# Kernel tuning notes

Hardware: AMD Instinct MI355X
Metric: run time of the kernel (lower is better)

The kernel has to match this reference:

```python
import jax, jax.numpy as jnp
import numpy as np

B, T, D = 8, 4096, 768

def setup_inputs() -> dict:
    key = jax.random.key(0)
    k1, k2, k3, k4, k5, k6 = jax.random.split(key, 6)
    inputs = jax.random.normal(k1, (B, T, D), dtype=jnp.float32)
    mask = jax.random.randint(k2, (B, T), 0, 2, dtype=jnp.int32)
    s = 1.0 / np.sqrt(D)
    Wq_w = jax.random.normal(k3, (D, D), dtype=jnp.float32) * s
    Wq_b = jax.random.normal(k4, (D,), dtype=jnp.float32) * 0.02
    Wk_w = jax.random.normal(k5, (D, D), dtype=jnp.float32) * s
    Wk_b = jax.random.normal(k6, (D,), dtype=jnp.float32) * 0.02
    return {"inputs": inputs, "mask": mask, "Wq_w": Wq_w, "Wq_b": Wq_b, "Wk_w": Wk_w, "Wk_b": Wk_b}

def reference(inputs, mask, Wq_w, Wq_b, Wk_w, Wk_b):
    # Linear layers (torch: x @ W.T + b)
    query = jnp.einsum('btd,ed->bte', inputs, Wq_w) + Wq_b  # (b,t,d)
    key = jnp.einsum('btd,ed->bte', inputs, Wk_w) + Wk_b    # (b,t,d)
    d_k = query.shape[-1]
    scores = jnp.einsum('bqd,bkd->bqk', query, key) / jnp.sqrt(jnp.float32(d_k))  # (b,t,t)
    # mask.unsqueeze(1): (b,1,t) broadcast over query rows
    scores = jnp.where(mask[:, None, :] == 0, jnp.float32(-1e9), scores)
    weights = jax.nn.softmax(scores, axis=2)  # (b,t,t)
    # einsum 'btd,btt->bd' == diagonal of weights, weighted sum of inputs
    w_diag = jnp.einsum('btt->bt', weights)   # (b,t)
    outputs = jnp.einsum('btd,bt->bd', inputs, w_diag)  # (b,d)
    return outputs
```

## Files before the change

### kernel.cpp

```cpp
#include <hip/hip_runtime.h>

#define BB 8
#define TT 4096
#define DD 768
#define MM (BB*TT)

typedef _Float16 f16;
typedef _Float16 f16x8 __attribute__((ext_vector_type(8)));
typedef float f32x4 __attribute__((ext_vector_type(4)));

typedef __attribute__((address_space(1))) void void_g;
typedef __attribute__((address_space(3))) void void_l;

__device__ __forceinline__ void gload16(const void* g, void* l) {
  __builtin_amdgcn_global_load_lds((void_g*)g, (void_l*)l, 16, 0, 0);
}

__global__ __launch_bounds__(256)
void compact_mask(const int* __restrict__ mask, int* __restrict__ idx,
                  int* __restrict__ nbv) {
  __shared__ int wcnt[4];
  const int b = blockIdx.x;
  const int w = threadIdx.x >> 6, l = threadIdx.x & 63;
  const int* mb = mask + b * TT + w * 1024;
  int mv[16];
  unsigned long long bal[16];
#pragma unroll
  for (int c = 0; c < 16; ++c) {
    mv[c] = mb[c * 64 + l];
    bal[c] = __ballot(mv[c] != 0);
  }
  int tot = 0;
#pragma unroll
  for (int c = 0; c < 16; ++c) tot += __popcll(bal[c]);
  if (l == 0) wcnt[w] = tot;
  __syncthreads();
  int base = 0;
  for (int ww = 0; ww < w; ++ww) base += wcnt[ww];
#pragma unroll
  for (int c = 0; c < 16; ++c) {
    const int pre = __popcll(bal[c] & ((1ull << l) - 1ull));
    if (mv[c]) idx[b * TT + base + pre] = w * 1024 + c * 64 + l;
    base += __popcll(bal[c]);
  }
  if (w == 3 && l == 0) nbv[b] = base;
}

__global__ __launch_bounds__(256)
void cvt2T(const float* __restrict__ a, const float* __restrict__ b,
           f16* __restrict__ oaT, f16* __restrict__ obT) {
  __shared__ float tile[64][65];
  const float* src = blockIdx.z ? b : a;
  f16* dst = blockIdx.z ? obT : oaT;
  const int n0 = blockIdx.x * 64, d0 = blockIdx.y * 64;
  const int r = threadIdx.x >> 6, c = threadIdx.x & 63;
#pragma unroll
  for (int k = 0; k < 16; ++k)
    tile[k * 4 + r][c] = src[(size_t)(n0 + k * 4 + r) * DD + d0 + c];
  __syncthreads();
#pragma unroll
  for (int k = 0; k < 16; ++k)
    dst[(size_t)(d0 + k * 4 + r) * DD + n0 + c] = (f16)tile[c][k * 4 + r];
}

__global__ __launch_bounds__(256)
void evec_k(const float* __restrict__ Wk, const float* __restrict__ bq,
            float* __restrict__ e) {
  const int d = blockIdx.x * 256 + threadIdx.x;
  float acc = 0.f;
  for (int n = 0; n < DD; ++n) acc += bq[n] * Wk[(size_t)n * DD + d];
  e[d] = acc;
}

__global__ __launch_bounds__(256)
void gather_cvt2(const float* __restrict__ X, const int* __restrict__ idx,
                 const int* __restrict__ nbv, const float* __restrict__ e,
                 f16* __restrict__ Xc, float* __restrict__ vb) {
  const int rr = blockIdx.x * 8 + (threadIdx.x >> 5);
  const int b = rr >> 12, j = rr & 4095;
  const int l = threadIdx.x & 31;
  if (j >= nbv[b]) return;
  const float scale = 0.036084391824351613f;
  const float* src = X + ((size_t)b * TT + idx[b * TT + j]) * DD + l * 24;
  f16* dst = Xc + ((size_t)b * TT + j) * DD + l * 24;
  const float* ep = e + l * 24;
  float vp = 0.f;
#pragma unroll
  for (int c = 0; c < 3; ++c) {
    float4 a = *(const float4*)(src + c * 8);
    float4 d4 = *(const float4*)(src + c * 8 + 4);
    f16x8 o;
    o[0] = (f16)a.x;  o[1] = (f16)a.y;  o[2] = (f16)a.z;  o[3] = (f16)a.w;
    o[4] = (f16)d4.x; o[5] = (f16)d4.y; o[6] = (f16)d4.z; o[7] = (f16)d4.w;
    *(f16x8*)(dst + c * 8) = o;
    vp += a.x * ep[c * 8]     + a.y * ep[c * 8 + 1] +
          a.z * ep[c * 8 + 2] + a.w * ep[c * 8 + 3] +
          d4.x * ep[c * 8 + 4] + d4.y * ep[c * 8 + 5] +
          d4.z * ep[c * 8 + 6] + d4.w * ep[c * 8 + 7];
  }
#pragma unroll
  for (int off = 1; off < 32; off <<= 1) vp += __shfl_xor(vp, off);
  if (l == 0) vb[b * TT + j] = vp * scale;
}

__global__ __launch_bounds__(256, 3)
void gemm_mt(const f16* __restrict__ WkT, const f16* __restrict__ WqT,
             f16* __restrict__ MT) {
  __shared__ f16 As[2][64 * 32];
  __shared__ f16 Ws[2][256 * 32];
  const int m0 = blockIdx.x * 64;
  const int n0 = blockIdx.y * 256;
  const int t = threadIdx.x;
  const int lane = t & 63;
  const int w = t >> 6;
  const int wn = w * 64;
  const int fr = lane & 15, fq = lane >> 4;
  const int xrd = ((fr >> 1) & 3) << 3;

  f32x4 acc[4][4] = {};

  const int r0 = t >> 2;
  const int c8 = ((t & 3) ^ ((t >> 3) & 3)) * 8;
  const f16* w0 = WqT + (size_t)(n0 + r0) * DD + c8;
  const f16* a0 = WkT + (size_t)(m0 + r0) * DD + c8;

#define PSTAGE(bf, ks_) do { \
    const int k0_ = (ks_) * 32; \
    gload16(a0 + k0_,                      &As[bf][w * 512]); \
    gload16(w0 + k0_,                      &Ws[bf][w * 512]); \
    gload16(w0 + (size_t)64  * DD + k0_,   &Ws[bf][2048 + w * 512]); \
    gload16(w0 + (size_t)128 * DD + k0_,   &Ws[bf][4096 + w * 512]); \
    gload16(w0 + (size_t)192 * DD + k0_,   &Ws[bf][6144 + w * 512]); \
  } while (0)

  PSTAGE(0, 0);
  __syncthreads();
  for (int ks = 0; ks < 24; ++ks) {
    const int bf = ks & 1;
    if (ks + 1 < 24) PSTAGE(bf ^ 1, ks + 1);
    f16x8 a[4], bfr[4];
#pragma unroll
    for (int i = 0; i < 4; ++i)
      a[i] = *(const f16x8*)&As[bf][(((i * 16 + fr) * 32) + fq * 8) ^ xrd];
#pragma unroll
    for (int j = 0; j < 4; ++j)
      bfr[j] = *(const f16x8*)&Ws[bf][(((wn + j * 16 + fr) * 32) + fq * 8) ^ xrd];
#pragma unroll
    for (int i = 0; i < 4; ++i)
#pragma unroll
      for (int j = 0; j < 4; ++j)
        acc[i][j] = __builtin_amdgcn_mfma_f32_16x16x32_f16(a[i], bfr[j], acc[i][j], 0, 0, 0);
    __syncthreads();
  }
#undef PSTAGE

#pragma unroll
  for (int j = 0; j < 4; ++j) {
    const int col = n0 + wn + j * 16 + fr;
#pragma unroll
    for (int i = 0; i < 4; ++i)
#pragma unroll
      for (int r = 0; r < 4; ++r) {
        const int row = m0 + i * 16 + fq * 4 + r;
        MT[(size_t)row * DD + col] = (f16)acc[i][j][r];
      }
  }
}

__global__ __launch_bounds__(256, 2)
void projY(const f16* __restrict__ Xc, const f16* __restrict__ MT,
           const int* __restrict__ nbv, f16* __restrict__ Yf) {
  const int b  = blockIdx.x >> 6;
  const int m0 = (blockIdx.x & 63) * 64;
  const int nb = nbv[b];
  if (m0 >= ((nb + 63) & ~63)) return;

  __shared__ f16 As[4][64 * 32];
  __shared__ f16 Ws[4][256 * 32];
  const int n0 = blockIdx.y * 256;
  const int t = threadIdx.x;
  const int lane = t & 63;
  const int w = t >> 6;
  const int wn = w * 64;
  const int fr = lane & 15, fq = lane >> 4;
  const int xrd = ((fr >> 1) & 3) << 3;

  f32x4 acc[4][4] = {};

  const int r0 = t >> 2;
  const int c8 = ((t & 3) ^ ((t >> 3) & 3)) * 8;
  const f16* w0 = MT + (size_t)(n0 + r0) * DD + c8;
  const f16* a0 = Xc + (size_t)b * TT * DD + (size_t)(m0 + r0) * DD + c8;

#define PSTAGE(sl, ks_) do { \
    const int k0_ = (ks_) * 32; \
    gload16(a0 + k0_,                      &As[sl][w * 512]); \
    gload16(w0 + k0_,                      &Ws[sl][w * 512]); \
    gload16(w0 + (size_t)64  * DD + k0_,   &Ws[sl][2048 + w * 512]); \
    gload16(w0 + (size_t)128 * DD + k0_,   &Ws[sl][4096 + w * 512]); \
    gload16(w0 + (size_t)192 * DD + k0_,   &Ws[sl][6144 + w * 512]); \
  } while (0)

  PSTAGE(0, 0);
  PSTAGE(1, 1);
  asm volatile("s_waitcnt vmcnt(5)" ::: "memory");
  __builtin_amdgcn_sched_barrier(0);
  __builtin_amdgcn_s_barrier();

  for (int ks = 0; ks < 24; ++ks) {
    const int sl = ks & 3;
    if (ks + 2 < 24) {
      PSTAGE((ks + 2) & 3, ks + 2);
      asm volatile("s_waitcnt vmcnt(10)" ::: "memory");
    } else if (ks + 1 < 24) {
      asm volatile("s_waitcnt vmcnt(5)" ::: "memory");
    } else {
      asm volatile("s_waitcnt vmcnt(0)" ::: "memory");
    }
    __builtin_amdgcn_sched_barrier(0);
    __builtin_amdgcn_s_barrier();
    __builtin_amdgcn_sched_barrier(0);

    f16x8 a[4], bfr[4];
#pragma unroll
    for (int i = 0; i < 4; ++i)
      a[i] = *(const f16x8*)&As[sl][(((i * 16 + fr) * 32) + fq * 8) ^ xrd];
#pragma unroll
    for (int j = 0; j < 4; ++j)
      bfr[j] = *(const f16x8*)&Ws[sl][(((wn + j * 16 + fr) * 32) + fq * 8) ^ xrd];
    __builtin_amdgcn_s_setprio(1);
#pragma unroll
    for (int i = 0; i < 4; ++i)
#pragma unroll
      for (int j = 0; j < 4; ++j)
        acc[i][j] = __builtin_amdgcn_mfma_f32_16x16x32_f16(a[i], bfr[j], acc[i][j], 0, 0, 0);
    __builtin_amdgcn_s_setprio(0);
    __builtin_amdgcn_sched_barrier(0);
    __builtin_amdgcn_s_barrier();
  }
#undef PSTAGE

#pragma unroll
  for (int j = 0; j < 4; ++j) {
    const int col = n0 + wn + j * 16 + fr;
#pragma unroll
    for (int i = 0; i < 4; ++i) {
#pragma unroll
      for (int r = 0; r < 4; ++r) {
        const int rowc = m0 + i * 16 + fq * 4 + r;
        const size_t q = (size_t)b * TT * DD +
            ((((size_t)(rowc >> 6) * 24 + (col >> 5)) * 4 + ((rowc >> 4) & 3)) * 512 +
             ((rowc & 15) + (((col >> 3) & 3) << 4)) * 8 + (col & 7));
        Yf[q] = (f16)acc[i][j][r];
      }
    }
  }
}

__global__ __launch_bounds__(256, 3)
void attn17b(const f16* __restrict__ Qf, const f16* __restrict__ K,
             const float* __restrict__ vbias, const int* __restrict__ nbv,
             float* __restrict__ pzv, float* __restrict__ sdg) {
  const int bid = blockIdx.x;
  const int qs = bid / 48;
  const int rem = bid % 48;
  const int kh = rem >> 3;
  const int bb = rem & 7;
  const int nb = nbv[bb];
  if (qs * 128 >= nb) return;

  __shared__ f16 Ks[2][128 * 64];
  const int t = threadIdx.x, l = t & 63, w = t >> 6;
  const int wq = w >> 1, wk = w & 1;
  const int fr = l & 15, fq = l >> 4;
  const int q0 = qs * 128;
  const float scale = 0.036084391824351613f;
  const int nkt = (nb + 127) >> 7;
  const int q6 = nkt / 6, r6 = nkt % 6;
  const int cnt = q6 + (kh < r6 ? 1 : 0);
  const int lo  = kh * q6 + (kh < r6 ? kh : r6);
  const int P = cnt * 12;

  const f16* Kg = K + (size_t)bb * TT * DD;
  const f16* qf = Qf + (size_t)bb * TT * DD + (size_t)(qs * 2 + wq) * 49152 + (size_t)l * 8;
  const float* vbp = vbias + bb * TT;

  const int c8 = ((t & 3) ^ ((t >> 3) & 3)) * 8;
  const f16* klo = Kg + (size_t)(t >> 2) * DD + c8;
  const f16* khi = klo + (size_t)64 * DD;

  const int sx = (fq ^ ((fr >> 1) & 3)) * 8;
  const int bbase = (wk * 64 + fr) * 32 + sx;

  f32x4 acc[4][4] = {};
  f32x4 zacc[4] = {};
  int im0 = 0, im1 = 0, im2 = 0, im3 = 0;
  float vb0 = 0.f, vb1 = 0.f, vb2 = 0.f, vb3 = 0.f;
  f16x8 avA[4], avB[4];

#define STAGE(bf, p_) do { \
    const size_t o0 = (size_t)(lo + (p_) / 12) * 128 * DD + (size_t)(((p_) % 12) * 64); \
    gload16(klo + o0,      &Ks[bf][w * 512]); \
    gload16(khi + o0,      &Ks[bf][2048 + w * 512]); \
    gload16(klo + o0 + 32, &Ks[bf][4096 + w * 512]); \
    gload16(khi + o0 + 32, &Ks[bf][6144 + w * 512]); \
  } while (0)

#define QLOAD(dst, dc_) do { \
    const f16* qp_ = qf + (size_t)(dc_) * 2048; \
    _Pragma("unroll") \
    for (int i = 0; i < 4; ++i) (dst)[i] = *(const f16x8*)(qp_ + i * 512); \
  } while (0)

#define MFMA_ALL(av_, bufv, off_) do { \
    f16x8 bv[4]; \
    _Pragma("unroll") \
    for (int j = 0; j < 4; ++j) bv[j] = *(const f16x8*)&Ks[bufv][(off_) + bbase + j * 512]; \
    __builtin_amdgcn_s_setprio(1); \
    _Pragma("unroll") \
    for (int i = 0; i < 4; ++i) \
      _Pragma("unroll") \
      for (int j = 0; j < 4; ++j) \
        acc[i][j] = __builtin_amdgcn_mfma_f32_16x16x32_f16((av_)[i], bv[j], acc[i][j], 0, 0, 0); \
    __builtin_amdgcn_s_setprio(0); \
  } while (0)

#define KT_EPILOGUE(kt_) do { \
    const float mb0 = im0 ? vb0 : -1e30f; \
    const float mb1 = im1 ? vb1 : -1e30f; \
    const float mb2 = im2 ? vb2 : -1e30f; \
    const float mb3 = im3 ? vb3 : -1e30f; \
    const bool isdiag = ((kt_) == qs); \
    _Pragma("unroll") \
    for (int i = 0; i < 4; ++i) { \
      _Pragma("unroll") \
      for (int rg = 0; rg < 4; ++rg) { \
        float v0 = fmaf(acc[i][0][rg], scale, mb0); \
        float v1 = fmaf(acc[i][1][rg], scale, mb1); \
        float v2 = fmaf(acc[i][2][rg], scale, mb2); \
        float v3 = fmaf(acc[i][3][rg], scale, mb3); \
        if (isdiag) { \
          const int rl = wq * 64 + i * 16 + fq * 4 + rg; \
          const int cl = wk * 64 + fr; \
          if (cl      == rl) sdg[(size_t)bb * TT + q0 + rl] = v0; \
          if (cl + 16 == rl) sdg[(size_t)bb * TT + q0 + rl] = v1; \
          if (cl + 32 == rl) sdg[(size_t)bb * TT + q0 + rl] = v2; \
          if (cl + 48 == rl) sdg[(size_t)bb * TT + q0 + rl] = v3; \
        } \
        zacc[i][rg] += __expf(v0) + __expf(v1) + __expf(v2) + __expf(v3); \
      } \
    } \
    _Pragma("unroll") \
    for (int i = 0; i < 4; ++i) \
      _Pragma("unroll") \
      for (int j = 0; j < 4; ++j) acc[i][j] = (f32x4)(0.f); \
  } while (0)

  STAGE(0, 0);
  QLOAD(avA, 0);
  __syncthreads();

  for (int p = 0; p < P; ++p) {
    const int buf = p & 1;
    const int kt = lo + p / 12, c = p % 12;
    if (c == 0) {
      const int cb0 = kt * 128 + wk * 64 + fr;
      im0 = (cb0 < nb); im1 = (cb0 + 16 < nb);
      im2 = (cb0 + 32 < nb); im3 = (cb0 + 48 < nb);
      vb0 = vbp[cb0]; vb1 = vbp[cb0 + 16];
      vb2 = vbp[cb0 + 32]; vb3 = vbp[cb0 + 48];
    }

    QLOAD(avB, 2 * c + 1);
    if (p + 1 < P) STAGE(buf ^ 1, p + 1);
    MFMA_ALL(avA, buf, 0);

    if (p + 1 < P) QLOAD(avA, 2 * (((p + 1) % 12)));
    MFMA_ALL(avB, buf, 4096);

    if (c == 11) KT_EPILOGUE(kt);

    __syncthreads();
  }
#undef STAGE
#undef QLOAD
#undef MFMA_ALL
#undef KT_EPILOGUE

  const int slot = kh * 2 + wk;
#pragma unroll
  for (int i = 0; i < 4; ++i) {
#pragma unroll
    for (int rg = 0; rg < 4; ++rg) {
      float z = zacc[i][rg];
#pragma unroll
      for (int off = 1; off < 16; off <<= 1) z += __shfl_xor(z, off);
      if (fr == 0) {
        const int row = wq * 64 + i * 16 + fq * 4 + rg;
        pzv[(size_t)slot * MM + bb * TT + q0 + row] = z;
      }
    }
  }
}

__global__ void merge12c(const float* __restrict__ pz, const float* __restrict__ sdg,
                         const int* __restrict__ nbv,
                         float* __restrict__ wdiagc, float* __restrict__ out) {
  int i = blockIdx.x * 256 + threadIdx.x;
  if (i < BB * DD) out[i] = 0.f;
  if (i >= MM) return;
  const int b = i >> 12, j = i & 4095;
  if (j >= nbv[b]) { wdiagc[i] = 0.f; return; }
  float Z = 0.f;
#pragma unroll
  for (int s = 0; s < 12; ++s) Z += pz[(size_t)s * MM + i];
  wdiagc[i] = __expf(sdg[i]) / Z;
}

__global__ __launch_bounds__(256)
void out_gemv_c(const f16* __restrict__ Xc, const float* __restrict__ wdiagc,
                const int* __restrict__ nbv, float* __restrict__ out) {
  __shared__ float wsm[256];
  const int b = blockIdx.z;
  const int nb = nbv[b];
  const int tbase = blockIdx.x * 256;
  if (tbase >= nb) return;
  const int d = blockIdx.y * 256 + threadIdx.x;
  wsm[threadIdx.x] = (tbase + threadIdx.x < nb) ? wdiagc[b * TT + tbase + threadIdx.x] : 0.f;
  __syncthreads();
  float acc = 0.f;
  const f16* xp = Xc + (size_t)(b * TT + tbase) * DD + d;
  const int lim = (nb - tbase < 256) ? (nb - tbase) : 256;
  for (int i = 0; i < lim; ++i) acc += (float)xp[(size_t)i * DD] * wsm[i];
  atomicAdd(&out[b * DD + d], acc);
}

extern "C" void kernel_launch(void* const* d_in, const int* in_sizes, int n_in,
                              void* d_out, int out_size, void* d_ws, size_t ws_size,
                              hipStream_t stream) {
  const float* X    = (const float*)d_in[0];
  const int*   mask = (const int*)d_in[1];
  const float* Wq_w = (const float*)d_in[2];
  const float* Wq_b = (const float*)d_in[3];
  const float* Wk_w = (const float*)d_in[4];
  const float* Wk_b = (const float*)d_in[5];
  float* out = (float*)d_out;

  const size_t n2 = (size_t)MM * DD;
  const size_t wde = (size_t)DD * DD;

  char* p = (char*)d_ws;
  f16* Yf  = (f16*)p;           p += n2 * sizeof(f16);
  f16* Xc  = (f16*)p;           p += n2 * sizeof(f16);
  f16* WqT = (f16*)p;           p += wde * sizeof(f16);
  f16* WkT = (f16*)p;           p += wde * sizeof(f16);
  f16* MT  = (f16*)p;           p += wde * sizeof(f16);
  float* ev = (float*)p;        p += DD * sizeof(float);
  int* idx = (int*)p;           p += (size_t)MM * sizeof(int);
  int* nbv = (int*)p;           p += 64;
  float* vb = (float*)p;        p += (size_t)MM * sizeof(float);
  float* pz = (float*)p;        p += (size_t)12 * MM * sizeof(float);
  float* sdg = (float*)p;       p += (size_t)MM * sizeof(float);
  float* wdiagc = (float*)p;    p += (size_t)MM * sizeof(float);

  compact_mask<<<8, 256, 0, stream>>>(mask, idx, nbv);
  cvt2T<<<dim3(12, 12, 2), 256, 0, stream>>>(Wq_w, Wk_w, WqT, WkT);
  evec_k<<<3, 256, 0, stream>>>(Wk_w, Wq_b, ev);
  gather_cvt2<<<4096, 256, 0, stream>>>(X, idx, nbv, ev, Xc, vb);
  gemm_mt<<<dim3(12, 3), 256, 0, stream>>>(WkT, WqT, MT);
  projY<<<dim3(512, 3), 256, 0, stream>>>(Xc, MT, nbv, Yf);
  attn17b<<<1536, 256, 0, stream>>>(Yf, Xc, vb, nbv, pz, sdg);
  merge12c<<<128, 256, 0, stream>>>(pz, sdg, nbv, wdiagc, out);
  out_gemv_c<<<dim3(16, 3, 8), 256, 0, stream>>>(Xc, wdiagc, nbv, out);
}
```

Baseline: 261.4 us.

## Merge prep kernels into fewer launches and simplify projY to double buffering

Folds the bias-vector GEMV into the mask-compaction kernel and the weight transpose into the gather/convert kernel, cutting four small launches down to two. projY drops from a 4-slot, 2-ahead prefetch pipeline with manual waitcnt and setprio to a plain 2-buffer scheme with __syncthreads, and raises its occupancy hint from 2 to 3 blocks. The fewer launches remove launch gaps. The simpler pipeline gives less latency hiding in exchange for lower LDS use and higher occupancy.

```diff
diff --git a/kernel.cpp b/kernel.cpp
--- a/kernel.cpp
+++ b/kernel.cpp
@@ -17,8 +17,16 @@
 }
 
 __global__ __launch_bounds__(256)
-void compact_mask(const int* __restrict__ mask, int* __restrict__ idx,
-                  int* __restrict__ nbv) {
+void compact_evec(const int* __restrict__ mask, int* __restrict__ idx,
+                  int* __restrict__ nbv, const float* __restrict__ Wk,
+                  const float* __restrict__ bq, float* __restrict__ e) {
+  if (blockIdx.x >= 8) {
+    const int d = (blockIdx.x - 8) * 256 + threadIdx.x;
+    float acc = 0.f;
+    for (int n = 0; n < DD; ++n) acc += bq[n] * Wk[(size_t)n * DD + d];
+    e[d] = acc;
+    return;
+  }
   __shared__ int wcnt[4];
   const int b = blockIdx.x;
   const int w = threadIdx.x >> 6, l = threadIdx.x & 63;
@@ -47,35 +55,28 @@
 }
 
 __global__ __launch_bounds__(256)
-void cvt2T(const float* __restrict__ a, const float* __restrict__ b,
-           f16* __restrict__ oaT, f16* __restrict__ obT) {
+void prep2(const float* __restrict__ X, const int* __restrict__ idx,
+           const int* __restrict__ nbv, const float* __restrict__ e,
+           f16* __restrict__ Xc, float* __restrict__ vb,
+           const float* __restrict__ Wq, const float* __restrict__ Wk,
+           f16* __restrict__ WqT, f16* __restrict__ WkT) {
   __shared__ float tile[64][65];
-  const float* src = blockIdx.z ? b : a;
-  f16* dst = blockIdx.z ? obT : oaT;
-  const int n0 = blockIdx.x * 64, d0 = blockIdx.y * 64;
-  const int r = threadIdx.x >> 6, c = threadIdx.x & 63;
-#pragma unroll
-  for (int k = 0; k < 16; ++k)
-    tile[k * 4 + r][c] = src[(size_t)(n0 + k * 4 + r) * DD + d0 + c];
-  __syncthreads();
-#pragma unroll
-  for (int k = 0; k < 16; ++k)
-    dst[(size_t)(d0 + k * 4 + r) * DD + n0 + c] = (f16)tile[c][k * 4 + r];
-}
-
-__global__ __launch_bounds__(256)
-void evec_k(const float* __restrict__ Wk, const float* __restrict__ bq,
-            float* __restrict__ e) {
-  const int d = blockIdx.x * 256 + threadIdx.x;
-  float acc = 0.f;
-  for (int n = 0; n < DD; ++n) acc += bq[n] * Wk[(size_t)n * DD + d];
-  e[d] = acc;
-}
-
-__global__ __launch_bounds__(256)
-void gather_cvt2(const float* __restrict__ X, const int* __restrict__ idx,
-                 const int* __restrict__ nbv, const float* __restrict__ e,
-                 f16* __restrict__ Xc, float* __restrict__ vb) {
+  if (blockIdx.x >= 4096) {
+    const int v = blockIdx.x - 4096;
+    const int bx = v % 12, by = (v / 12) % 12, bz = v / 144;
+    const float* src = bz ? Wk : Wq;
+    f16* dst = bz ? WkT : WqT;
+    const int n0 = bx * 64, d0 = by * 64;
+    const int r = threadIdx.x >> 6, c = threadIdx.x & 63;
+#pragma unroll
+    for (int k = 0; k < 16; ++k)
+      tile[k * 4 + r][c] = src[(size_t)(n0 + k * 4 + r) * DD + d0 + c];
+    __syncthreads();
+#pragma unroll
+    for (int k = 0; k < 16; ++k)
+      dst[(size_t)(d0 + k * 4 + r) * DD + n0 + c] = (f16)tile[c][k * 4 + r];
+    return;
+  }
   const int rr = blockIdx.x * 8 + (threadIdx.x >> 5);
   const int b = rr >> 12, j = rr & 4095;
   const int l = threadIdx.x & 31;
@@ -167,7 +168,7 @@
   }
 }
 
-__global__ __launch_bounds__(256, 2)
+__global__ __launch_bounds__(256, 3)
 void projY(const f16* __restrict__ Xc, const f16* __restrict__ MT,
            const int* __restrict__ nbv, f16* __restrict__ Yf) {
   const int b  = blockIdx.x >> 6;
@@ -175,8 +176,8 @@
   const int nb = nbv[b];
   if (m0 >= ((nb + 63) & ~63)) return;
 
-  __shared__ f16 As[4][64 * 32];
-  __shared__ f16 Ws[4][256 * 32];
+  __shared__ f16 As[2][64 * 32];
+  __shared__ f16 Ws[2][256 * 32];
   const int n0 = blockIdx.y * 256;
   const int t = threadIdx.x;
   const int lane = t & 63;
@@ -192,51 +193,33 @@
   const f16* w0 = MT + (size_t)(n0 + r0) * DD + c8;
   const f16* a0 = Xc + (size_t)b * TT * DD + (size_t)(m0 + r0) * DD + c8;
 
-#define PSTAGE(sl, ks_) do { \
+#define PSTAGE(bf, ks_) do { \
     const int k0_ = (ks_) * 32; \
-    gload16(a0 + k0_,                      &As[sl][w * 512]); \
-    gload16(w0 + k0_,                      &Ws[sl][w * 512]); \
-    gload16(w0 + (size_t)64  * DD + k0_,   &Ws[sl][2048 + w * 512]); \
-    gload16(w0 + (size_t)128 * DD + k0_,   &Ws[sl][4096 + w * 512]); \
-    gload16(w0 + (size_t)192 * DD + k0_,   &Ws[sl][6144 + w * 512]); \
+    gload16(a0 + k0_,                      &As[bf][w * 512]); \
+    gload16(w0 + k0_,                      &Ws[bf][w * 512]); \
+    gload16(w0 + (size_t)64  * DD + k0_,   &Ws[bf][2048 + w * 512]); \
+    gload16(w0 + (size_t)128 * DD + k0_,   &Ws[bf][4096 + w * 512]); \
+    gload16(w0 + (size_t)192 * DD + k0_,   &Ws[bf][6144 + w * 512]); \
   } while (0)
 
   PSTAGE(0, 0);
-  PSTAGE(1, 1);
-  asm volatile("s_waitcnt vmcnt(5)" ::: "memory");
-  __builtin_amdgcn_sched_barrier(0);
-  __builtin_amdgcn_s_barrier();
-
+  __syncthreads();
   for (int ks = 0; ks < 24; ++ks) {
-    const int sl = ks & 3;
-    if (ks + 2 < 24) {
-      PSTAGE((ks + 2) & 3, ks + 2);
-      asm volatile("s_waitcnt vmcnt(10)" ::: "memory");
-    } else if (ks + 1 < 24) {
-      asm volatile("s_waitcnt vmcnt(5)" ::: "memory");
-    } else {
-      asm volatile("s_waitcnt vmcnt(0)" ::: "memory");
-    }
-    __builtin_amdgcn_sched_barrier(0);
-    __builtin_amdgcn_s_barrier();
-    __builtin_amdgcn_sched_barrier(0);
-
+    const int bf = ks & 1;
+    if (ks + 1 < 24) PSTAGE(bf ^ 1, ks + 1);
     f16x8 a[4], bfr[4];
 #pragma unroll
     for (int i = 0; i < 4; ++i)
-      a[i] = *(const f16x8*)&As[sl][(((i * 16 + fr) * 32) + fq * 8) ^ xrd];
+      a[i] = *(const f16x8*)&As[bf][(((i * 16 + fr) * 32) + fq * 8) ^ xrd];
 #pragma unroll
     for (int j = 0; j < 4; ++j)
-      bfr[j] = *(const f16x8*)&Ws[sl][(((wn + j * 16 + fr) * 32) + fq * 8) ^ xrd];
-    __builtin_amdgcn_s_setprio(1);
+      bfr[j] = *(const f16x8*)&Ws[bf][(((wn + j * 16 + fr) * 32) + fq * 8) ^ xrd];
 #pragma unroll
     for (int i = 0; i < 4; ++i)
 #pragma unroll
       for (int j = 0; j < 4; ++j)
         acc[i][j] = __builtin_amdgcn_mfma_f32_16x16x32_f16(a[i], bfr[j], acc[i][j], 0, 0, 0);
-    __builtin_amdgcn_s_setprio(0);
-    __builtin_amdgcn_sched_barrier(0);
-    __builtin_amdgcn_s_barrier();
+    __syncthreads();
   }
 #undef PSTAGE
 
@@ -445,6 +428,7 @@
   const float* Wk_w = (const float*)d_in[4];
   const float* Wk_b = (const float*)d_in[5];
   float* out = (float*)d_out;
+  (void)Wk_b;
 
   const size_t n2 = (size_t)MM * DD;
   const size_t wde = (size_t)DD * DD;
@@ -463,10 +447,9 @@
   float* sdg = (float*)p;       p += (size_t)MM * sizeof(float);
   float* wdiagc = (float*)p;    p += (size_t)MM * sizeof(float);
 
-  compact_mask<<<8, 256, 0, stream>>>(mask, idx, nbv);
-  cvt2T<<<dim3(12, 12, 2), 256, 0, stream>>>(Wq_w, Wk_w, WqT, WkT);
-  evec_k<<<3, 256, 0, stream>>>(Wk_w, Wq_b, ev);
-  gather_cvt2<<<4096, 256, 0, stream>>>(X, idx, nbv, ev, Xc, vb);
+  compact_evec<<<11, 256, 0, stream>>>(mask, idx, nbv, Wk_w, Wq_b, ev);
+  prep2<<<4384, 256, 0, stream>>>(X, idx, nbv, ev, Xc, vb,
+                                  Wq_w, Wk_w, WqT, WkT);
   gemm_mt<<<dim3(12, 3), 256, 0, stream>>>(WkT, WqT, MT);
   projY<<<dim3(512, 3), 256, 0, stream>>>(Xc, MT, nbv, Yf);
   attn17b<<<1536, 256, 0, stream>>>(Yf, Xc, vb, nbv, pz, sdg);
```

New measurement: 247.2 us. 5.4% less time.
